# Kernel tuning notes

Hardware: AMD Instinct MI355X
Metric: run time of the kernel (lower is better)

## Reference

```python
import jax, jax.numpy as jnp
import numpy as np

NUM_EMBEDDINGS = 1024
EMBEDDING_DIM = 256
COMMITMENT_COST = 0.25


def setup_inputs() -> dict:
    key = jax.random.key(0)
    k1, k2 = jax.random.split(key)
    z_e = jax.random.normal(k1, (64, EMBEDDING_DIM, 32, 32), dtype=jnp.float32)
    # codebook init: uniform(-1/K, 1/K), matching nn.Embedding init in the module
    emb = jax.random.uniform(k2, (NUM_EMBEDDINGS, EMBEDDING_DIM), dtype=jnp.float32,
                             minval=-1.0 / NUM_EMBEDDINGS, maxval=1.0 / NUM_EMBEDDINGS)
    return {"z_e": z_e, "emb": emb}


def reference(z_e, emb):
    B, D, H, W = z_e.shape
    K = emb.shape[0]
    z = jnp.transpose(z_e, (0, 2, 3, 1))          # [B,H,W,D]
    x = z.reshape(-1, D)                           # [N,D], N = B*H*W
    dists = (jnp.sum(x * x, axis=1, keepdims=True)
             + jnp.sum(emb * emb, axis=1)[None, :]
             - 2.0 * (x @ emb.T))
    idx = jnp.argmin(dists, axis=1)                # [N] int
    z_q = emb[idx].reshape(z.shape)                # [B,H,W,D]
    e_latent_loss = jnp.mean((jax.lax.stop_gradient(z_q) - z) ** 2)
    q_latent_loss = jnp.mean((z_q - jax.lax.stop_gradient(z)) ** 2)
    loss = q_latent_loss + COMMITMENT_COST * e_latent_loss
    # straight-through estimator
    z_q_st = z + jax.lax.stop_gradient(z_q - z)
    counts = jnp.bincount(idx, length=K).astype(z.dtype)
    avg_probs = counts / jnp.asarray(x.shape[0], z.dtype)
    perplexity = jnp.exp(-jnp.sum(avg_probs * jnp.log(avg_probs + 1e-10)))
    return jnp.transpose(z_q_st, (0, 3, 1, 2)), loss, perplexity, idx
```

## Files before the change

kernel.cpp:

```cpp
#include <hip/hip_runtime.h>
#include <hip/hip_fp16.h>
#include <stdint.h>


#define D_DIM   256
#define K_CODES 1024
#define N_ROWS  65536
#define N_ELEM  16777216
#define IDX_OFF 16777218
#define FLAG_MARGIN 1.5e-4f
#define AMB_CAP 65536
#define A_SCALE 16.0f
#define B_SCALE 4096.0f
#define INV_SCALE2 3.0517578125e-05f

typedef short short8 __attribute__((ext_vector_type(8)));
typedef _Float16 half8 __attribute__((ext_vector_type(8)));
typedef float f32x4  __attribute__((ext_vector_type(4)));

__device__ __forceinline__ unsigned int mono(float s) {
    unsigned int u = __float_as_uint(s);
    return (u & 0x80000000u) ? ~u : (u | 0x80000000u);
}
__device__ __forceinline__ float unmono(unsigned int u) {
    return __uint_as_float((u & 0x80000000u) ? (u & 0x7FFFFFFFu) : ~u);
}
__device__ __forceinline__ unsigned short f16_rne(float x) {
    return __half_as_ushort(__float2half(x));
}
__device__ __forceinline__ void gld16(const void* g, void* l) {
    __builtin_amdgcn_global_load_lds(
        (const __attribute__((address_space(1))) unsigned int*)g,
        (__attribute__((address_space(3))) unsigned int*)l, 16, 0, 0);
}

__launch_bounds__(128)
__global__ void a_prep_kernel(const float* __restrict__ z_e,
                              unsigned short* __restrict__ A_hi,
                              float* __restrict__ xnorm) {
#pragma clang fp contract(off)
    __shared__ float T[32][257];
    __shared__ float H[32][2];
    const int tid = threadIdx.x;
    const int bx = blockIdx.x;
    const int b = bx >> 5, hw0 = (bx & 31) << 5;
    const float* zb = z_e + (size_t)b * 262144 + hw0;
    #pragma unroll 4
    for (int it = 0; it < 16; ++it) {
        int flat = it * 128 + tid;
        int d = flat >> 3;
        int hw4 = (flat & 7) << 2;
        float4 v = *(const float4*)(zb + (size_t)d * 1024 + hw4);
        T[hw4 + 0][d] = v.x; T[hw4 + 1][d] = v.y;
        T[hw4 + 2][d] = v.z; T[hw4 + 3][d] = v.w;
    }
    __syncthreads();
    if (tid < 64) {
        int row = tid >> 1, h = tid & 1;
        const float* q = &T[row][h * 128];
        float r[8];
        #pragma unroll
        for (int j = 0; j < 8; ++j) { float x = q[j]; r[j] = x * x; }
        for (int i = 8; i < 128; i += 8)
            #pragma unroll
            for (int j = 0; j < 8; ++j) { float x = q[i + j]; r[j] = r[j] + x * x; }
        H[row][h] = ((r[0] + r[1]) + (r[2] + r[3])) + ((r[4] + r[5]) + (r[6] + r[7]));
    }
    __syncthreads();
    if (tid < 32) xnorm[b * 1024 + hw0 + tid] = H[tid][0] + H[tid][1];
    {
        int row = tid >> 2, seg = tid & 3;
        const float* src = &T[row][seg * 64];
        unsigned short* dst = A_hi + ((size_t)(b * 1024 + hw0 + row) * 256 + seg * 64);
        #pragma unroll
        for (int c = 0; c < 8; ++c) {
            unsigned int ub[4];
            #pragma unroll
            for (int p = 0; p < 4; ++p) {
                unsigned int lo = f16_rne(src[c * 8 + 2 * p] * A_SCALE);
                unsigned int hi = f16_rne(src[c * 8 + 2 * p + 1] * A_SCALE);
                ub[p] = lo | (hi << 16);
            }
            *(uint4*)(dst + c * 8) = make_uint4(ub[0], ub[1], ub[2], ub[3]);
        }
    }
}

__launch_bounds__(256)
__global__ void emb_prep_kernel(const float* __restrict__ emb,
                                float* __restrict__ enorm,
                                unsigned short* __restrict__ B_hi,
                                float* __restrict__ embT) {
#pragma clang fp contract(off)
    const int k = blockIdx.x * 256 + threadIdx.x;
    const float* p = emb + (size_t)k * D_DIM;
    float half[2];
    #pragma unroll
    for (int h = 0; h < 2; ++h) {
        const float* q = p + h * 128;
        float r[8];
        #pragma unroll
        for (int j = 0; j < 8; ++j) { float x = q[j]; r[j] = x * x; }
        for (int i = 8; i < 128; i += 8)
            #pragma unroll
            for (int j = 0; j < 8; ++j) { float x = q[i + j]; r[j] = r[j] + x * x; }
        half[h] = ((r[0] + r[1]) + (r[2] + r[3])) + ((r[4] + r[5]) + (r[6] + r[7]));
    }
    enorm[k] = half[0] + half[1];
    unsigned int* dst = (unsigned int*)(B_hi + (size_t)k * D_DIM);
    for (int d = 0; d < 128; ++d) {
        unsigned int lo = f16_rne(p[2 * d] * B_SCALE);
        unsigned int hi = f16_rne(p[2 * d + 1] * B_SCALE);
        dst[d] = lo | (hi << 16);
    }
    for (int d = 0; d < D_DIM; ++d)
        embT[(size_t)d * K_CODES + k] = p[d];
}

__launch_bounds__(256, 2)
__global__ void dist2_kernel(const unsigned short* __restrict__ A_hi,
                             const unsigned short* __restrict__ B_hi,
                             const float* __restrict__ xnorm,
                             const float* __restrict__ enorm,
                             int* __restrict__ fidx,
                             int* __restrict__ amb,
                             int* __restrict__ amb_count) {
    __shared__ __align__(16) char smem[81920];
    unsigned long long* red = (unsigned long long*)(smem + 65536);

    const int tid  = threadIdx.x;
    const int lane = tid & 63, w = tid >> 6;
    const int quad = lane >> 4, l16 = lane & 15;
    const int wr = w >> 1, wc = w & 1;
    const int row0 = blockIdx.x * 128;

    const int aq    = (((lane & 3) ^ ((lane >> 3) & 3)) << 3);
    const int arsub = (w << 4) + (lane >> 2);
    const int rdoff = ((quad ^ ((l16 >> 1) & 3)) << 4);

    #pragma unroll
    for (int t = 0; t < 16; ++t) {
        const int arow = ((t & 1) << 6) + arsub;
        const int s    = t >> 1;
        gld16(A_hi + (((size_t)(row0 + arow)) << 8) + s * 32 + aq,
              smem + t * 4096 + w * 1024);
    }
    gld16(B_hi + (((size_t)(arsub)) << 8) + aq,       smem + 65536 + w * 1024);
    gld16(B_hi + (((size_t)(64 + arsub)) << 8) + aq,  smem + 65536 + 4096 + w * 1024);
    __syncthreads();

    float xnr[4][4];
    #pragma unroll
    for (int i = 0; i < 4; ++i)
        #pragma unroll
        for (int r = 0; r < 4; ++r)
            xnr[i][r] = xnorm[row0 + wr * 64 + i * 16 + quad * 4 + r];

    const float INF = __uint_as_float(0x7F800000u);
    float m1[4][4], m2[4][4];
    unsigned int ix[4][4];
    #pragma unroll
    for (int i = 0; i < 4; ++i)
        #pragma unroll
        for (int r = 0; r < 4; ++r) { m1[i][r] = INF; m2[i][r] = INF; ix[i][r] = 0u; }

    int cur = 0;
    for (int cb = 0; cb < 8; ++cb) {
        f32x4 acc[4][4];
        #pragma unroll
        for (int i = 0; i < 4; ++i)
            #pragma unroll
            for (int j = 0; j < 4; ++j) acc[i][j] = (f32x4){0.f, 0.f, 0.f, 0.f};

        for (int s = 0; s < 8; ++s) {
            const int nstep = cb * 8 + s + 1;
            if (nstep < 64) {
                const int ncb = nstep >> 3, ns = nstep & 7;
                char* nb = smem + 65536 + ((cur ^ 1) << 13);
                gld16(B_hi + (((size_t)(ncb * 128 + arsub)) << 8) + ns * 32 + aq,
                      nb + w * 1024);
                gld16(B_hi + (((size_t)(ncb * 128 + 64 + arsub)) << 8) + ns * 32 + aq,
                      nb + 4096 + w * 1024);
            }
            const char* bb = smem + 65536 + (cur << 13);
            half8 af[4], bf[4];
            #pragma unroll
            for (int i = 0; i < 4; ++i)
                af[i] = *(const half8*)(smem + s * 8192 + (wr * 64 + i * 16 + l16) * 64 + rdoff);
            #pragma unroll
            for (int j = 0; j < 4; ++j)
                bf[j] = *(const half8*)(bb + (wc * 64 + j * 16 + l16) * 64 + rdoff);
            #pragma unroll
            for (int i = 0; i < 4; ++i)
                #pragma unroll
                for (int j = 0; j < 4; ++j)
                    acc[i][j] = __builtin_amdgcn_mfma_f32_16x16x32_f16(af[i], bf[j], acc[i][j], 0, 0, 0);
            __syncthreads();
            cur ^= 1;
        }

        float enj[4];
        #pragma unroll
        for (int j = 0; j < 4; ++j) enj[j] = enorm[cb * 128 + wc * 64 + j * 16 + l16];
        #pragma unroll
        for (int i = 0; i < 4; ++i) {
            #pragma unroll
            for (int r = 0; r < 4; ++r) {
                const float xn = xnr[i][r];
                float a = m1[i][r], b = m2[i][r];
                unsigned int id = ix[i][r];
                #pragma unroll
                for (int j = 0; j < 4; ++j) {
                    const unsigned int n = cb * 128 + wc * 64 + j * 16 + l16;
                    float sc = fmaf(acc[i][j][r], -INV_SCALE2, xn + enj[j]);
                    bool c = sc < a;
                    b = fminf(b, fmaxf(a, sc));
                    a = fminf(a, sc);
                    id = c ? n : id;
                }
                m1[i][r] = a; m2[i][r] = b; ix[i][r] = id;
            }
        }
    }

    #pragma unroll
    for (int i = 0; i < 4; ++i) {
        #pragma unroll
        for (int r = 0; r < 4; ++r) {
            unsigned long long a1 = ((unsigned long long)mono(m1[i][r]) << 32) | ix[i][r];
            unsigned long long a2 = ((unsigned long long)mono(m2[i][r]) << 32) | 0xFFFFFFFFull;
            #pragma unroll
            for (int m = 1; m < 16; m <<= 1) {
                unsigned long long q1 = __shfl_xor(a1, m, 16);
                unsigned long long q2 = __shfl_xor(a2, m, 16);
                if (q1 < a1) { a2 = (a1 < q2) ? a1 : q2; a1 = q1; }
                else         { a2 = (a2 < q1) ? a2 : q1; }
            }
            if (l16 == 0) {
                int rowl = wr * 64 + i * 16 + quad * 4 + r;
                red[(rowl * 2 + wc) * 2 + 0] = a1;
                red[(rowl * 2 + wc) * 2 + 1] = a2;
            }
        }
    }
    __syncthreads();
    if (tid < 128) {
        unsigned long long a1 = red[(tid * 2 + 0) * 2 + 0];
        unsigned long long a2 = red[(tid * 2 + 0) * 2 + 1];
        unsigned long long b1 = red[(tid * 2 + 1) * 2 + 0];
        unsigned long long b2 = red[(tid * 2 + 1) * 2 + 1];
        if (b1 < a1) { a2 = (a1 < b2) ? a1 : b2; a1 = b1; }
        else         { a2 = (a2 < b1) ? a2 : b1; }
        const int row = row0 + tid;
        fidx[row] = (int)(a1 & 0xFFFFFFFFull);
        float s1 = unmono((unsigned int)(a1 >> 32));
        float s2 = unmono((unsigned int)(a2 >> 32));
        if (s2 - s1 <= FLAG_MARGIN) {
            int slot = atomicAdd(amb_count, 1);
            if (slot < AMB_CAP) amb[slot] = row;
        }
    }
}

__launch_bounds__(256)
__global__ void rescue4_kernel(const float* __restrict__ z_e,
                               const float* __restrict__ embT,
                               const float* __restrict__ xnorm,
                               const float* __restrict__ enorm,
                               const int* __restrict__ amb,
                               const int* __restrict__ amb_count,
                               int* __restrict__ fidx) {
    __shared__ float xs[4][256];
    __shared__ int rows[4];
    __shared__ unsigned long long pm[4][257];
    const int tid = threadIdx.x;
    int cnt = *amb_count;
    if (cnt > AMB_CAP) cnt = AMB_CAP;
    if (cnt <= 0) return;
    const int ngroups = (cnt + 3) >> 2;
    for (int g = blockIdx.x; g < ngroups; g += gridDim.x) {
        if (tid < 4) {
            int e = g * 4 + tid;
            rows[tid] = amb[e < cnt ? e : (cnt - 1)];
        }
        __syncthreads();
        {
            const int j = tid >> 6, d0 = (tid & 63) * 4;
            const int row = rows[j];
            const int b = row >> 10, hw = row & 1023;
            const float* zp = z_e + (size_t)b * 262144 + hw;
            #pragma unroll
            for (int i = 0; i < 4; ++i)
                xs[j][d0 + i] = zp[(size_t)(d0 + i) * 1024];
        }
        __syncthreads();

        double acc[4][4];
        #pragma unroll
        for (int c = 0; c < 4; ++c)
            #pragma unroll
            for (int j = 0; j < 4; ++j) acc[c][j] = 0.0;

        const float* ep = embT + 4 * tid;
        for (int d0 = 0; d0 < D_DIM; d0 += 8) {
            float4 ev[8];
            #pragma unroll
            for (int u = 0; u < 8; ++u)
                ev[u] = *(const float4*)(ep + (size_t)(d0 + u) * K_CODES);
            #pragma unroll
            for (int u = 0; u < 8; ++u) {
                const int d = d0 + u;
                double e0 = (double)ev[u].x, e1 = (double)ev[u].y;
                double e2 = (double)ev[u].z, e3 = (double)ev[u].w;
                double x0 = (double)xs[0][d], x1 = (double)xs[1][d];
                double x2 = (double)xs[2][d], x3 = (double)xs[3][d];
                acc[0][0] += x0 * e0; acc[0][1] += x1 * e0; acc[0][2] += x2 * e0; acc[0][3] += x3 * e0;
                acc[1][0] += x0 * e1; acc[1][1] += x1 * e1; acc[1][2] += x2 * e1; acc[1][3] += x3 * e1;
                acc[2][0] += x0 * e2; acc[2][1] += x1 * e2; acc[2][2] += x2 * e2; acc[2][3] += x3 * e2;
                acc[3][0] += x0 * e3; acc[3][1] += x1 * e3; acc[3][2] += x2 * e3; acc[3][3] += x3 * e3;
            }
        }

        float xnr[4];
        #pragma unroll
        for (int j = 0; j < 4; ++j) xnr[j] = xnorm[rows[j]];

        unsigned long long mm[4] = {~0ull, ~0ull, ~0ull, ~0ull};
        #pragma unroll
        for (int c = 0; c < 4; ++c) {
            const int k = 4 * tid + c;
            const float en = enorm[k];
            #pragma unroll
            for (int j = 0; j < 4; ++j) {
                float dv = (float)acc[c][j];
                float t = xnr[j] + en;
                float s = t - 2.f * dv;
                unsigned long long p = ((unsigned long long)mono(s) << 32) | (unsigned int)k;
                if (p < mm[j]) mm[j] = p;
            }
        }
        #pragma unroll
        for (int j = 0; j < 4; ++j) pm[j][tid] = mm[j];
        __syncthreads();
        for (int s = 128; s > 0; s >>= 1) {
            if (tid < s) {
                #pragma unroll
                for (int j = 0; j < 4; ++j)
                    if (pm[j][tid + s] < pm[j][tid]) pm[j][tid] = pm[j][tid + s];
            }
            __syncthreads();
        }
        if (tid < 4) fidx[rows[tid]] = (int)(pm[tid][0] & 0xFFFFFFFFull);
        __syncthreads();
    }
}

__global__ void epilogue_kernel(const float* __restrict__ z_e,
                                const float* __restrict__ emb,
                                const int* __restrict__ fidx,
                                float* __restrict__ out,
                                int* __restrict__ counts,
                                float* __restrict__ loss_sum) {
    __shared__ int   kb[64];
    __shared__ float rs[256];
    const int tid = threadIdx.x;
    const int rcb = blockIdx.x;
    const int b   = rcb >> 4;
    const int hw0 = (rcb & 15) << 6;

    if (tid < 64) {
        int k = fidx[rcb * 64 + tid];
        kb[tid] = k;
        out[(size_t)IDX_OFF + (size_t)rcb * 64 + tid] = (float)k;
        atomicAdd(&counts[k], 1);
    }
    __syncthreads();

    const int j4 = (tid & 15) << 2;
    const int dq = tid >> 4;
    const float* e0 = emb + (size_t)kb[j4 + 0] * D_DIM;
    const float* e1 = emb + (size_t)kb[j4 + 1] * D_DIM;
    const float* e2 = emb + (size_t)kb[j4 + 2] * D_DIM;
    const float* e3 = emb + (size_t)kb[j4 + 3] * D_DIM;
    const size_t base = (size_t)b * 262144 + hw0 + j4;
    float ls = 0.f;
    #pragma unroll 4
    for (int d = dq; d < D_DIM; d += 16) {
        size_t off = base + ((size_t)d << 10);
        float4 x = *(const float4*)(z_e + off);
        float4 q;
        q.x = e0[d]; q.y = e1[d]; q.z = e2[d]; q.w = e3[d];
        *(float4*)(out + off) = q;
        float d0 = q.x - x.x, d1 = q.y - x.y, d2 = q.z - x.z, d3 = q.w - x.w;
        ls += d0 * d0; ls += d1 * d1; ls += d2 * d2; ls += d3 * d3;
    }
    rs[tid] = ls;
    __syncthreads();
    for (int s = 128; s > 0; s >>= 1) {
        if (tid < s) rs[tid] += rs[tid + s];
        __syncthreads();
    }
    if (tid == 0) atomicAdd(loss_sum, rs[0]);
}

__global__ void finalize_kernel(const int* __restrict__ counts,
                                const float* __restrict__ loss_sum,
                                float* __restrict__ out) {
    __shared__ float rs[256];
    const int tid = threadIdx.x;
    float s = 0.f;
    for (int k = tid; k < K_CODES; k += 256) {
        float p = (float)counts[k] / 65536.0f;
        s += p * logf(p + 1e-10f);
    }
    rs[tid] = s;
    __syncthreads();
    for (int st = 128; st > 0; st >>= 1) {
        if (tid < st) rs[tid] += rs[tid + st];
        __syncthreads();
    }
    if (tid == 0) {
        out[N_ELEM]     = loss_sum[0] * 1.25f / 16777216.0f;
        out[N_ELEM + 1] = expf(-rs[0]);
    }
}

extern "C" void kernel_launch(void* const* d_in, const int* in_sizes, int n_in,
                              void* d_out, int out_size, void* d_ws, size_t ws_size,
                              hipStream_t stream) {
    const float* z_e = (const float*)d_in[0];
    const float* emb = (const float*)d_in[1];
    float* out = (float*)d_out;
    char*  ws  = (char*)d_ws;

    unsigned short* A_hi = (unsigned short*)d_out;

    float*          enorm    = (float*)ws;
    float*          xnorm    = (float*)(ws + 4096);
    int*            fidx     = (int*)(ws + 266240);
    int*            counts   = (int*)(ws + 528384);
    float*          loss_sum = (float*)(ws + 532480);
    int*            amb_cnt  = (int*)(ws + 532484);
    int*            amb      = (int*)(ws + 532488);
    unsigned short* B_hi     = (unsigned short*)(ws + 794752);
    float*          embT     = (float*)(ws + 1319040);

    hipMemsetAsync(counts, 0, 4104, stream);

    a_prep_kernel<<<2048, 128, 0, stream>>>(z_e, A_hi, xnorm);
    emb_prep_kernel<<<K_CODES / 256, 256, 0, stream>>>(emb, enorm, B_hi, embT);
    dist2_kernel<<<512, 256, 0, stream>>>(A_hi, B_hi, xnorm, enorm, fidx, amb, amb_cnt);
    rescue4_kernel<<<1024, 256, 0, stream>>>(z_e, embT, xnorm, enorm, amb, amb_cnt, fidx);
    epilogue_kernel<<<N_ROWS / 64, 256, 0, stream>>>(z_e, emb, fidx, out, counts, loss_sum);
    finalize_kernel<<<1, 256, 0, stream>>>(counts, loss_sum, out);
}
```

Baseline: 322.3 us.

## Fuse A/embedding prep and memset into one kernel, add MFMA priority hints

Merges the activation-prep kernel, the embedding-prep kernel and the hipMemsetAsync into a single launch. The first four blocks handle codebook norms, fp16 conversion and the transpose, now reading through vectorized float4 loads. The remaining blocks do the z_e transpose and fp16 conversion with 256 threads each instead of 128. It also wraps the MFMA inner loop in s_setprio hints. The intent is to remove launch and memset overhead and the slow scalar per-thread embedding prep; the four embedding blocks could end up as stragglers.

```diff
diff --git a/kernel.cpp b/kernel.cpp
--- a/kernel.cpp
+++ b/kernel.cpp
@@ -34,20 +34,81 @@
         (__attribute__((address_space(3))) unsigned int*)l, 16, 0, 0);
 }
 
-__launch_bounds__(128)
-__global__ void a_prep_kernel(const float* __restrict__ z_e,
-                              unsigned short* __restrict__ A_hi,
-                              float* __restrict__ xnorm) {
+__launch_bounds__(256)
+__global__ void prep_kernel(const float* __restrict__ z_e,
+                            const float* __restrict__ emb,
+                            unsigned short* __restrict__ A_hi,
+                            float* __restrict__ xnorm,
+                            float* __restrict__ enorm,
+                            unsigned short* __restrict__ B_hi,
+                            float* __restrict__ embT,
+                            int* __restrict__ counts,
+                            float* __restrict__ loss_sum,
+                            int* __restrict__ amb_count) {
 #pragma clang fp contract(off)
     __shared__ float T[32][257];
     __shared__ float H[32][2];
     const int tid = threadIdx.x;
-    const int bx = blockIdx.x;
+    const int bid = blockIdx.x;
+
+    if (bid < 4) {
+        const int k = bid * 256 + tid;
+        counts[k] = 0;
+        if (bid == 0 && tid == 0) { *loss_sum = 0.f; *amb_count = 0; }
+        const float* p = emb + (size_t)k * D_DIM;
+        unsigned int* dstB = (unsigned int*)(B_hi + (size_t)k * D_DIM);
+        float halfv[2];
+        #pragma unroll
+        for (int h = 0; h < 2; ++h) {
+            float r[8];
+            #pragma unroll
+            for (int qq = 0; qq < 2; ++qq) {
+                float4 ev[16];
+                const float* qb = p + h * 128 + qq * 64;
+                #pragma unroll
+                for (int m = 0; m < 16; ++m)
+                    ev[m] = *(const float4*)(qb + 4 * m);
+                #pragma unroll
+                for (int t = 0; t < 8; ++t) {
+                    const float4 a = ev[2 * t], b = ev[2 * t + 1];
+                    if (qq == 0 && t == 0) {
+                        r[0] = a.x * a.x; r[1] = a.y * a.y; r[2] = a.z * a.z; r[3] = a.w * a.w;
+                        r[4] = b.x * b.x; r[5] = b.y * b.y; r[6] = b.z * b.z; r[7] = b.w * b.w;
+                    } else {
+                        r[0] += a.x * a.x; r[1] += a.y * a.y; r[2] += a.z * a.z; r[3] += a.w * a.w;
+                        r[4] += b.x * b.x; r[5] += b.y * b.y; r[6] += b.z * b.z; r[7] += b.w * b.w;
+                    }
+                }
+                #pragma unroll
+                for (int m = 0; m < 16; m += 2) {
+                    const float4 a = ev[m], b = ev[m + 1];
+                    unsigned int u0 = f16_rne(a.x * B_SCALE) | ((unsigned int)f16_rne(a.y * B_SCALE) << 16);
+                    unsigned int u1 = f16_rne(a.z * B_SCALE) | ((unsigned int)f16_rne(a.w * B_SCALE) << 16);
+                    unsigned int u2 = f16_rne(b.x * B_SCALE) | ((unsigned int)f16_rne(b.y * B_SCALE) << 16);
+                    unsigned int u3 = f16_rne(b.z * B_SCALE) | ((unsigned int)f16_rne(b.w * B_SCALE) << 16);
+                    *(uint4*)(dstB + (h * 64 + qq * 32 + 2 * m)) = make_uint4(u0, u1, u2, u3);
+                }
+                const int dbase = h * 128 + qq * 64;
+                #pragma unroll
+                for (int m = 0; m < 16; ++m) {
+                    embT[(size_t)(dbase + 4 * m + 0) * K_CODES + k] = ev[m].x;
+                    embT[(size_t)(dbase + 4 * m + 1) * K_CODES + k] = ev[m].y;
+                    embT[(size_t)(dbase + 4 * m + 2) * K_CODES + k] = ev[m].z;
+                    embT[(size_t)(dbase + 4 * m + 3) * K_CODES + k] = ev[m].w;
+                }
+            }
+            halfv[h] = ((r[0] + r[1]) + (r[2] + r[3])) + ((r[4] + r[5]) + (r[6] + r[7]));
+        }
+        enorm[k] = halfv[0] + halfv[1];
+        return;
+    }
+
+    const int bx = bid - 4;
     const int b = bx >> 5, hw0 = (bx & 31) << 5;
     const float* zb = z_e + (size_t)b * 262144 + hw0;
     #pragma unroll 4
-    for (int it = 0; it < 16; ++it) {
-        int flat = it * 128 + tid;
+    for (int it = 0; it < 8; ++it) {
+        int flat = it * 256 + tid;
         int d = flat >> 3;
         int hw4 = (flat & 7) << 2;
         float4 v = *(const float4*)(zb + (size_t)d * 1024 + hw4);
@@ -69,11 +130,11 @@
     __syncthreads();
     if (tid < 32) xnorm[b * 1024 + hw0 + tid] = H[tid][0] + H[tid][1];
     {
-        int row = tid >> 2, seg = tid & 3;
-        const float* src = &T[row][seg * 64];
-        unsigned short* dst = A_hi + ((size_t)(b * 1024 + hw0 + row) * 256 + seg * 64);
-        #pragma unroll
-        for (int c = 0; c < 8; ++c) {
+        int row = tid >> 3, seg8 = tid & 7;
+        const float* src = &T[row][seg8 * 32];
+        unsigned short* dst = A_hi + ((size_t)(b * 1024 + hw0 + row) * 256 + seg8 * 32);
+        #pragma unroll
+        for (int c = 0; c < 4; ++c) {
             unsigned int ub[4];
             #pragma unroll
             for (int p = 0; p < 4; ++p) {
@@ -84,37 +145,6 @@
             *(uint4*)(dst + c * 8) = make_uint4(ub[0], ub[1], ub[2], ub[3]);
         }
     }
-}
-
-__launch_bounds__(256)
-__global__ void emb_prep_kernel(const float* __restrict__ emb,
-                                float* __restrict__ enorm,
-                                unsigned short* __restrict__ B_hi,
-                                float* __restrict__ embT) {
-#pragma clang fp contract(off)
-    const int k = blockIdx.x * 256 + threadIdx.x;
-    const float* p = emb + (size_t)k * D_DIM;
-    float half[2];
-    #pragma unroll
-    for (int h = 0; h < 2; ++h) {
-        const float* q = p + h * 128;
-        float r[8];
-        #pragma unroll
-        for (int j = 0; j < 8; ++j) { float x = q[j]; r[j] = x * x; }
-        for (int i = 8; i < 128; i += 8)
-            #pragma unroll
-            for (int j = 0; j < 8; ++j) { float x = q[i + j]; r[j] = r[j] + x * x; }
-        half[h] = ((r[0] + r[1]) + (r[2] + r[3])) + ((r[4] + r[5]) + (r[6] + r[7]));
-    }
-    enorm[k] = half[0] + half[1];
-    unsigned int* dst = (unsigned int*)(B_hi + (size_t)k * D_DIM);
-    for (int d = 0; d < 128; ++d) {
-        unsigned int lo = f16_rne(p[2 * d] * B_SCALE);
-        unsigned int hi = f16_rne(p[2 * d + 1] * B_SCALE);
-        dst[d] = lo | (hi << 16);
-    }
-    for (int d = 0; d < D_DIM; ++d)
-        embT[(size_t)d * K_CODES + k] = p[d];
 }
 
 __launch_bounds__(256, 2)
@@ -190,11 +220,13 @@
             #pragma unroll
             for (int j = 0; j < 4; ++j)
                 bf[j] = *(const half8*)(bb + (wc * 64 + j * 16 + l16) * 64 + rdoff);
+            __builtin_amdgcn_s_setprio(1);
             #pragma unroll
             for (int i = 0; i < 4; ++i)
                 #pragma unroll
                 for (int j = 0; j < 4; ++j)
                     acc[i][j] = __builtin_amdgcn_mfma_f32_16x16x32_f16(af[i], bf[j], acc[i][j], 0, 0, 0);
+            __builtin_amdgcn_s_setprio(0);
             __syncthreads();
             cur ^= 1;
         }
@@ -445,10 +477,8 @@
     unsigned short* B_hi     = (unsigned short*)(ws + 794752);
     float*          embT     = (float*)(ws + 1319040);
 
-    hipMemsetAsync(counts, 0, 4104, stream);
-
-    a_prep_kernel<<<2048, 128, 0, stream>>>(z_e, A_hi, xnorm);
-    emb_prep_kernel<<<K_CODES / 256, 256, 0, stream>>>(emb, enorm, B_hi, embT);
+    prep_kernel<<<2052, 256, 0, stream>>>(z_e, emb, A_hi, xnorm, enorm, B_hi, embT,
+                                          counts, loss_sum, amb_cnt);
     dist2_kernel<<<512, 256, 0, stream>>>(A_hi, B_hi, xnorm, enorm, fidx, amb, amb_cnt);
     rescue4_kernel<<<1024, 256, 0, stream>>>(z_e, embT, xnorm, enorm, amb, amb_cnt, fidx);
     epilogue_kernel<<<N_ROWS / 64, 256, 0, stream>>>(z_e, emb, fidx, out, counts, loss_sum);
```

New measurement: 281.8 us. -12.6%, faster.
